# Kernel tuning notes

Measured on AMD Instinct MI355X. Metric: run time of the kernel, lower is better.

## Reference

```python
import jax, jax.numpy as jnp
import numpy as np

B, N, C, E = 4, 20000, 64, 320000

def setup_inputs() -> dict:
    key = jax.random.key(0)
    ks = jax.random.split(key, 9)
    s = 0.1
    return {
        "x": jax.random.normal(ks[0], (B, N, C), jnp.float32),
        "edge_index": jax.random.randint(ks[1], (2, E), 0, N, jnp.int64),
        "lin_w": jax.random.normal(ks[2], (C, C), jnp.float32) * s,
        "bias": jnp.zeros((C,), jnp.float32),
        "up1_w": jax.random.normal(ks[3], (C, C), jnp.float32) * s,
        "up2_w": jax.random.normal(ks[4], (C, C), jnp.float32) * s,
        "lo1_w": jax.random.normal(ks[5], (C, C), jnp.float32) * s,
        "lo2_w": jax.random.normal(ks[6], (C, C), jnp.float32) * s,
        "last_w": jax.random.normal(ks[7], (2 * C, 2 * C), jnp.float32) * s,
    }

def reference(x, edge_index, lin_w, bias, up1_w, up2_w, lo1_w, lo2_w, last_w):
    n = x.shape[1]
    # add self loops (PyG add_self_loops)
    loops = jnp.arange(n, dtype=edge_index.dtype)
    row = jnp.concatenate([edge_index[0], loops])  # source
    col = jnp.concatenate([edge_index[1], loops])  # target
    # linear transform (Linear with no bias: x @ W^T)
    h = jnp.einsum("bnc,oc->bno", x, lin_w)
    # symmetric degree normalization; degree computed on col (targets)
    deg = jax.ops.segment_sum(jnp.ones_like(col, dtype=h.dtype), col, num_segments=n)
    dis = jnp.where(deg > 0, deg ** -0.5, 0.0)
    norm = dis[row] * dis[col]  # [E+N]
    # gather / scale / scatter-add (GCN propagate with aggr='add')
    msg = h[:, row, :] * norm[None, :, None]          # [B, E+N, C]
    agg = jax.ops.segment_sum(jnp.swapaxes(msg, 0, 1), col, num_segments=n)  # [N, B, C]
    out = jnp.swapaxes(agg, 0, 1) + bias              # [B, N, C]
    fst = jax.nn.sigmoid(out)
    upper = jnp.einsum("bnc,oc->bno", jnp.einsum("bnc,oc->bno", fst, up1_w), up2_w)
    lower = jnp.einsum("bnc,oc->bno", jnp.einsum("bnc,oc->bno", fst, lo1_w), lo2_w)
    combined = jnp.concatenate([upper, lower], axis=2)  # [B, N, 2C]
    last = jnp.einsum("bnc,oc->bno", combined, last_w)
    return jax.nn.relu(last)
```

## Files before the change

kernel.cpp:

```cpp
#include <hip/hip_runtime.h>
#include <cstdint>
#include <cstddef>

#define NODES 20000
#define NEDGE 320000
#define CAP 64
#define NEB 1250
#define LINB 16
#define BIGB 32

using bf16x8 = __attribute__((ext_vector_type(8))) __bf16;
using f32x4  = __attribute__((ext_vector_type(4))) float;
using f32x2  = __attribute__((ext_vector_type(2))) float;

__device__ __forceinline__ unsigned short f2bf(float f) {
  union { float f; unsigned int u; } v; v.f = f;
  unsigned int r = v.u + 0x7FFF + ((v.u >> 16) & 1);
  return (unsigned short)(r >> 16);
}

__global__ void k_build(const int* __restrict__ ei, int* __restrict__ cnt,
                        int* __restrict__ csr,
                        const float* __restrict__ lin, const float* __restrict__ u1,
                        const float* __restrict__ u2, const float* __restrict__ l1,
                        const float* __restrict__ l2, const float* __restrict__ lastw,
                        unsigned short* __restrict__ wb16) {
  __shared__ float tmp_u[4][64];
  __shared__ float tmp_l[4][64];
  int bid = blockIdx.x, t = threadIdx.x;
  if (bid < NEB) {
    int i = bid * 256 + t;
    if (i < NEDGE) {
      int row = ei[i];
      int col = ei[NEDGE + i];
      int pos = atomicAdd(&cnt[col], 1);
      if (pos < CAP) csr[col * CAP + pos] = row;
    }
  } else if (bid < NEB + LINB) {
    int g = (bid - NEB) * 256 + t;
    wb16[g] = f2bf(lin[g]);
  } else {
    int o0 = (bid - NEB - LINB) * 4;
    int ol = t >> 6, p = t & 63;
    float su = 0.f, sl = 0.f;
    for (int k = 0; k < 64; ++k) {
      float lu = lastw[(o0 + ol) * 128 + k];
      float ll = lastw[(o0 + ol) * 128 + 64 + k];
      su += lu * u2[k * 64 + p];
      sl += ll * l2[k * 64 + p];
    }
    tmp_u[ol][p] = su;
    tmp_l[ol][p] = sl;
    __syncthreads();
    int j = p;
    float acc = 0.f;
    for (int q = 0; q < 64; ++q)
      acc += tmp_u[ol][q] * u1[q * 64 + j] + tmp_l[ol][q] * l1[q * 64 + j];
    wb16[4096 + (o0 + ol) * 64 + j] = f2bf(acc);
  }
}

__global__ void k_xconv(const int* __restrict__ cnt, float* __restrict__ dis,
                        const float* __restrict__ x, unsigned int* __restrict__ xs8) {
  int g = blockIdx.x * 256 + threadIdx.x;
  int n = g >> 6, i = g & 63;
  int b = i >> 4, c = (i & 15) * 4;
  float ds = rsqrtf((float)(cnt[n] + 1));
  if (i == 0) dis[n] = ds;
  f32x4 v = __builtin_nontemporal_load(
      (const f32x4*)(x + ((size_t)b * NODES + n) * 64 + c));
  int p = 0;
  p = __builtin_amdgcn_cvt_pk_fp8_f32(v.x * ds, v.y * ds, p, false);
  p = __builtin_amdgcn_cvt_pk_fp8_f32(v.z * ds, v.w * ds, p, true);
  xs8[(size_t)n * 64 + i] = (unsigned int)p;
}

__global__ __launch_bounds__(256) void k_gpost(const int* __restrict__ cnt,
                                               const int* __restrict__ csr,
                                               const unsigned int* __restrict__ xs8,
                                               const float* __restrict__ dis,
                                               const float* __restrict__ bias,
                                               const unsigned short* __restrict__ wb16,
                                               float* __restrict__ out) {
  __shared__ unsigned short xa[64][72];
  __shared__ unsigned short fst[64][72];
  int t = threadIdx.x;
  int w = t >> 6, l = t & 63;
  int n0 = blockIdx.x * 16;

  for (int j = 0; j < 4; ++j) {
    int n = n0 + 4 * w + j;
    int dn = cnt[n]; if (dn > CAP) dn = CAP;
    int beg = n * CAP, end = beg + dn;
    float a0, a1, a2, a3;
    {
      unsigned int u = xs8[(size_t)n * 64 + l];
      f32x2 lo = __builtin_amdgcn_cvt_pk_f32_fp8(u, false);
      f32x2 hi = __builtin_amdgcn_cvt_pk_f32_fp8(u, true);
      a0 = lo.x; a1 = lo.y; a2 = hi.x; a3 = hi.y;
    }
    int i = beg;
    for (; i + 8 <= end; i += 8) {
      int r0 = csr[i],     r1 = csr[i + 1], r2 = csr[i + 2], r3 = csr[i + 3];
      int r4 = csr[i + 4], r5 = csr[i + 5], r6 = csr[i + 6], r7 = csr[i + 7];
      unsigned int u0 = xs8[(size_t)r0 * 64 + l];
      unsigned int u1 = xs8[(size_t)r1 * 64 + l];
      unsigned int u2 = xs8[(size_t)r2 * 64 + l];
      unsigned int u3 = xs8[(size_t)r3 * 64 + l];
      unsigned int u4 = xs8[(size_t)r4 * 64 + l];
      unsigned int u5 = xs8[(size_t)r5 * 64 + l];
      unsigned int u6 = xs8[(size_t)r6 * 64 + l];
      unsigned int u7 = xs8[(size_t)r7 * 64 + l];
#pragma unroll
      for (int e = 0; e < 8; ++e) {
        unsigned int u = e == 0 ? u0 : e == 1 ? u1 : e == 2 ? u2 : e == 3 ? u3
                       : e == 4 ? u4 : e == 5 ? u5 : e == 6 ? u6 : u7;
        f32x2 lo = __builtin_amdgcn_cvt_pk_f32_fp8(u, false);
        f32x2 hi = __builtin_amdgcn_cvt_pk_f32_fp8(u, true);
        a0 += lo.x; a1 += lo.y; a2 += hi.x; a3 += hi.y;
      }
    }
    for (; i < end; ++i) {
      unsigned int u = xs8[(size_t)csr[i] * 64 + l];
      f32x2 lo = __builtin_amdgcn_cvt_pk_f32_fp8(u, false);
      f32x2 hi = __builtin_amdgcn_cvt_pk_f32_fp8(u, true);
      a0 += lo.x; a1 += lo.y; a2 += hi.x; a3 += hi.y;
    }
    ushort4 o;
    o.x = f2bf(a0); o.y = f2bf(a1); o.z = f2bf(a2); o.w = f2bf(a3);
    *(ushort4*)&xa[16 * w + 4 * j + (l >> 4)][(l & 15) * 4] = o;
  }
  __syncthreads();

  int m = l & 15, q = l >> 4;
  const unsigned short* wlin = wb16;
  const unsigned short* bigw = wb16 + 4096;

  {
    f32x4 acc1[4] = {{0,0,0,0},{0,0,0,0},{0,0,0,0},{0,0,0,0}};
#pragma unroll
    for (int kk = 0; kk < 2; ++kk) {
      bf16x8 a = *(const bf16x8*)(wlin + (16 * w + m) * 64 + q * 8 + 32 * kk);
#pragma unroll
      for (int nt = 0; nt < 4; ++nt) {
        bf16x8 b = *(const bf16x8*)&xa[16 * nt + m][q * 8 + 32 * kk];
        acc1[nt] = __builtin_amdgcn_mfma_f32_16x16x32_bf16(a, b, acc1[nt], 0, 0, 0);
      }
    }
    float4 b4 = *(const float4*)(bias + 16 * w + 4 * q);
#pragma unroll
    for (int nt = 0; nt < 4; ++nt) {
      int row = 16 * nt + m;
      float ds = dis[n0 + (row >> 2)];
      float v0 = acc1[nt][0] * ds + b4.x;
      float v1 = acc1[nt][1] * ds + b4.y;
      float v2 = acc1[nt][2] * ds + b4.z;
      float v3 = acc1[nt][3] * ds + b4.w;
      ushort4 o;
      o.x = f2bf(1.f / (1.f + __expf(-v0)));
      o.y = f2bf(1.f / (1.f + __expf(-v1)));
      o.z = f2bf(1.f / (1.f + __expf(-v2)));
      o.w = f2bf(1.f / (1.f + __expf(-v3)));
      *(ushort4*)&fst[row][16 * w + 4 * q] = o;
    }
  }
  __syncthreads();

  {
    f32x4 acc2[2][4] = {{{0,0,0,0},{0,0,0,0},{0,0,0,0},{0,0,0,0}},
                        {{0,0,0,0},{0,0,0,0},{0,0,0,0},{0,0,0,0}}};
#pragma unroll
    for (int kk = 0; kk < 2; ++kk) {
#pragma unroll
      for (int nt = 0; nt < 4; ++nt) {
        bf16x8 a = *(const bf16x8*)&fst[16 * nt + m][q * 8 + 32 * kk];
#pragma unroll
        for (int mt = 0; mt < 2; ++mt) {
          bf16x8 b = *(const bf16x8*)(bigw + (32 * w + 16 * mt + m) * 64 + q * 8 + 32 * kk);
          acc2[mt][nt] = __builtin_amdgcn_mfma_f32_16x16x32_bf16(a, b, acc2[mt][nt], 0, 0, 0);
        }
      }
    }
#pragma unroll
    for (int mt = 0; mt < 2; ++mt)
#pragma unroll
      for (int nt = 0; nt < 4; ++nt)
#pragma unroll
        for (int r = 0; r < 4; ++r) {
          int row = 16 * nt + 4 * q + r;
          int n = n0 + (row >> 2), b = row & 3;
          float v = acc2[mt][nt][r];
          __builtin_nontemporal_store(
              v > 0.f ? v : 0.f,
              out + ((size_t)b * NODES + n) * 128 + 32 * w + 16 * mt + m);
        }
  }
}

extern "C" void kernel_launch(void* const* d_in, const int* in_sizes, int n_in,
                              void* d_out, int out_size, void* d_ws, size_t ws_size,
                              hipStream_t stream) {
  const float* x     = (const float*)d_in[0];
  const int*   ei    = (const int*)d_in[1];
  const float* lin_w = (const float*)d_in[2];
  const float* bias  = (const float*)d_in[3];
  const float* up1   = (const float*)d_in[4];
  const float* up2   = (const float*)d_in[5];
  const float* lo1   = (const float*)d_in[6];
  const float* lo2   = (const float*)d_in[7];
  const float* lastw = (const float*)d_in[8];
  float* out = (float*)d_out;

  char* ws = (char*)d_ws;
  unsigned short* wb16 = (unsigned short*)(ws);
  float* dis        = (float*)(ws + (64 << 10));
  int*   cnt        = (int*)(ws + (192 << 10));
  int*   csr        = (int*)(ws + (1 << 20));
  unsigned int* xs8 = (unsigned int*)(ws + (8 << 20));

  (void)hipMemsetAsync(cnt, 0, NODES * sizeof(int), stream);
  k_build<<<NEB + LINB + BIGB, 256, 0, stream>>>(ei, cnt, csr, lin_w, up1, up2,
                                                 lo1, lo2, lastw, wb16);
  k_xconv<<<NODES / 4, 256, 0, stream>>>(cnt, dis, x, xs8);
  k_gpost<<<NODES / 16, 256, 0, stream>>>(cnt, csr, xs8, dis, bias, wb16, out);
}
```

Measured before the change: 146.3 us.

## Fold x fp8 conversion into build kernel and apply source normalization in gather

Moves the fp8 conversion of x into the graph-build launch, so it no longer has to wait for the degree counts, and removes the separate conversion kernel and the dis buffer. The source-node normalization is now applied inside the gather by reading cnt[r] for every neighbour and computing rsqrt there. This saves one kernel launch and its serialization, at the cost of extra random cnt loads and rsqrt work in the gather loop. The fp8 values are no longer prescaled, so quantization happens before normalization, which slightly changes the rounding.

```diff
diff --git a/kernel.cpp b/kernel.cpp
--- a/kernel.cpp
+++ b/kernel.cpp
@@ -8,6 +8,7 @@
 #define NEB 1250
 #define LINB 16
 #define BIGB 32
+#define XB   5000
 
 using bf16x8 = __attribute__((ext_vector_type(8))) __bf16;
 using f32x4  = __attribute__((ext_vector_type(4))) float;
@@ -20,7 +21,8 @@
 }
 
 __global__ void k_build(const int* __restrict__ ei, int* __restrict__ cnt,
-                        int* __restrict__ csr,
+                        int* __restrict__ csr, const float* __restrict__ x,
+                        unsigned int* __restrict__ xs8,
                         const float* __restrict__ lin, const float* __restrict__ u1,
                         const float* __restrict__ u2, const float* __restrict__ l1,
                         const float* __restrict__ l2, const float* __restrict__ lastw,
@@ -36,11 +38,21 @@
       int pos = atomicAdd(&cnt[col], 1);
       if (pos < CAP) csr[col * CAP + pos] = row;
     }
-  } else if (bid < NEB + LINB) {
+  } else if (bid < NEB + XB) {
     int g = (bid - NEB) * 256 + t;
+    int n = g >> 6, i = g & 63;
+    int b = i >> 4, c = (i & 15) * 4;
+    f32x4 v = __builtin_nontemporal_load(
+        (const f32x4*)(x + ((size_t)b * NODES + n) * 64 + c));
+    int p = 0;
+    p = __builtin_amdgcn_cvt_pk_fp8_f32(v.x, v.y, p, false);
+    p = __builtin_amdgcn_cvt_pk_fp8_f32(v.z, v.w, p, true);
+    xs8[(size_t)n * 64 + i] = (unsigned int)p;
+  } else if (bid < NEB + XB + LINB) {
+    int g = (bid - NEB - XB) * 256 + t;
     wb16[g] = f2bf(lin[g]);
   } else {
-    int o0 = (bid - NEB - LINB) * 4;
+    int o0 = (bid - NEB - XB - LINB) * 4;
     int ol = t >> 6, p = t & 63;
     float su = 0.f, sl = 0.f;
     for (int k = 0; k < 64; ++k) {
@@ -60,25 +72,9 @@
   }
 }
 
-__global__ void k_xconv(const int* __restrict__ cnt, float* __restrict__ dis,
-                        const float* __restrict__ x, unsigned int* __restrict__ xs8) {
-  int g = blockIdx.x * 256 + threadIdx.x;
-  int n = g >> 6, i = g & 63;
-  int b = i >> 4, c = (i & 15) * 4;
-  float ds = rsqrtf((float)(cnt[n] + 1));
-  if (i == 0) dis[n] = ds;
-  f32x4 v = __builtin_nontemporal_load(
-      (const f32x4*)(x + ((size_t)b * NODES + n) * 64 + c));
-  int p = 0;
-  p = __builtin_amdgcn_cvt_pk_fp8_f32(v.x * ds, v.y * ds, p, false);
-  p = __builtin_amdgcn_cvt_pk_fp8_f32(v.z * ds, v.w * ds, p, true);
-  xs8[(size_t)n * 64 + i] = (unsigned int)p;
-}
-
 __global__ __launch_bounds__(256) void k_gpost(const int* __restrict__ cnt,
                                                const int* __restrict__ csr,
                                                const unsigned int* __restrict__ xs8,
-                                               const float* __restrict__ dis,
                                                const float* __restrict__ bias,
                                                const unsigned short* __restrict__ wb16,
                                                float* __restrict__ out) {
@@ -90,14 +86,16 @@
 
   for (int j = 0; j < 4; ++j) {
     int n = n0 + 4 * w + j;
-    int dn = cnt[n]; if (dn > CAP) dn = CAP;
+    int cv = cnt[n];
+    int dn = cv > CAP ? CAP : cv;
+    float dsn = rsqrtf((float)(cv + 1));
     int beg = n * CAP, end = beg + dn;
     float a0, a1, a2, a3;
     {
       unsigned int u = xs8[(size_t)n * 64 + l];
       f32x2 lo = __builtin_amdgcn_cvt_pk_f32_fp8(u, false);
       f32x2 hi = __builtin_amdgcn_cvt_pk_f32_fp8(u, true);
-      a0 = lo.x; a1 = lo.y; a2 = hi.x; a3 = hi.y;
+      a0 = dsn * lo.x; a1 = dsn * lo.y; a2 = dsn * hi.x; a3 = dsn * hi.y;
     }
     int i = beg;
     for (; i + 8 <= end; i += 8) {
@@ -111,20 +109,27 @@
       unsigned int u5 = xs8[(size_t)r5 * 64 + l];
       unsigned int u6 = xs8[(size_t)r6 * 64 + l];
       unsigned int u7 = xs8[(size_t)r7 * 64 + l];
+      int c0 = cnt[r0], c1 = cnt[r1], c2 = cnt[r2], c3 = cnt[r3];
+      int c4 = cnt[r4], c5 = cnt[r5], c6 = cnt[r6], c7 = cnt[r7];
 #pragma unroll
       for (int e = 0; e < 8; ++e) {
         unsigned int u = e == 0 ? u0 : e == 1 ? u1 : e == 2 ? u2 : e == 3 ? u3
                        : e == 4 ? u4 : e == 5 ? u5 : e == 6 ? u6 : u7;
+        int cc = e == 0 ? c0 : e == 1 ? c1 : e == 2 ? c2 : e == 3 ? c3
+               : e == 4 ? c4 : e == 5 ? c5 : e == 6 ? c6 : c7;
+        float d = rsqrtf((float)(cc + 1));
         f32x2 lo = __builtin_amdgcn_cvt_pk_f32_fp8(u, false);
         f32x2 hi = __builtin_amdgcn_cvt_pk_f32_fp8(u, true);
-        a0 += lo.x; a1 += lo.y; a2 += hi.x; a3 += hi.y;
+        a0 += d * lo.x; a1 += d * lo.y; a2 += d * hi.x; a3 += d * hi.y;
       }
     }
     for (; i < end; ++i) {
-      unsigned int u = xs8[(size_t)csr[i] * 64 + l];
+      int r = csr[i];
+      unsigned int u = xs8[(size_t)r * 64 + l];
+      float d = rsqrtf((float)(cnt[r] + 1));
       f32x2 lo = __builtin_amdgcn_cvt_pk_f32_fp8(u, false);
       f32x2 hi = __builtin_amdgcn_cvt_pk_f32_fp8(u, true);
-      a0 += lo.x; a1 += lo.y; a2 += hi.x; a3 += hi.y;
+      a0 += d * lo.x; a1 += d * lo.y; a2 += d * hi.x; a3 += d * hi.y;
     }
     ushort4 o;
     o.x = f2bf(a0); o.y = f2bf(a1); o.z = f2bf(a2); o.w = f2bf(a3);
@@ -151,7 +156,8 @@
 #pragma unroll
     for (int nt = 0; nt < 4; ++nt) {
       int row = 16 * nt + m;
-      float ds = dis[n0 + (row >> 2)];
+      int n = n0 + (row >> 2);
+      float ds = rsqrtf((float)(cnt[n] + 1));
       float v0 = acc1[nt][0] * ds + b4.x;
       float v1 = acc1[nt][1] * ds + b4.y;
       float v2 = acc1[nt][2] * ds + b4.z;
@@ -213,14 +219,12 @@
 
   char* ws = (char*)d_ws;
   unsigned short* wb16 = (unsigned short*)(ws);
-  float* dis        = (float*)(ws + (64 << 10));
   int*   cnt        = (int*)(ws + (192 << 10));
   int*   csr        = (int*)(ws + (1 << 20));
   unsigned int* xs8 = (unsigned int*)(ws + (8 << 20));
 
   (void)hipMemsetAsync(cnt, 0, NODES * sizeof(int), stream);
-  k_build<<<NEB + LINB + BIGB, 256, 0, stream>>>(ei, cnt, csr, lin_w, up1, up2,
-                                                 lo1, lo2, lastw, wb16);
-  k_xconv<<<NODES / 4, 256, 0, stream>>>(cnt, dis, x, xs8);
-  k_gpost<<<NODES / 16, 256, 0, stream>>>(cnt, csr, xs8, dis, bias, wb16, out);
-}
+  k_build<<<NEB + XB + LINB + BIGB, 256, 0, stream>>>(ei, cnt, csr, x, xs8, lin_w,
+                                                      up1, up2, lo1, lo2, lastw, wb16);
+  k_gpost<<<NODES / 16, 256, 0, stream>>>(cnt, csr, xs8, bias, wb16, out);
+}
```

After: 155.6 us. 6.4% more time.
